# Performance work log

Measured on AMD Instinct MI355X. Metric: run time of the kernel, lower is better.

The kernel has to match this reference:

```python
import jax, jax.numpy as jnp
import numpy as np

N = 50000          # nodes
E_RAND = 590000    # random edges (+ N self-loops -> E = 640000)
IN_F = 128
OUT_F = 128
H, D = 8, 16       # num_heads, head_dim (H*D == OUT_F)
HOP = 5
ALPHA = 0.1
SLOPE = 0.2
EPS = 1e-5


def _layer_norm(x, g, b):
    mu = jnp.mean(x, axis=-1, keepdims=True)
    var = jnp.mean((x - mu) ** 2, axis=-1, keepdims=True)
    return (x - mu) * jax.lax.rsqrt(var + EPS) * g + b


def setup_inputs() -> dict:
    key = jax.random.key(0)
    ks = jax.random.split(key, 10)
    loops = jnp.arange(N, dtype=jnp.int32)  # self-loops -> no 0-in-degree nodes
    src = jnp.concatenate([loops, jax.random.randint(ks[0], (E_RAND,), 0, N, dtype=jnp.int32)])
    dst = jnp.concatenate([loops, jax.random.randint(ks[1], (E_RAND,), 0, N, dtype=jnp.int32)])
    s = 0.05  # xavier-like small init gain
    return {
        "feat": jax.random.normal(ks[2], (N, IN_F), jnp.float32),
        "src": src,
        "dst": dst,
        "w_head": jax.random.normal(ks[3], (OUT_F, IN_F), jnp.float32) * s,
        "w_tail": jax.random.normal(ks[4], (OUT_F, IN_F), jnp.float32) * s,
        "w_ent": jax.random.normal(ks[5], (OUT_F, IN_F), jnp.float32) * s,
        "attn": jax.random.normal(ks[6], (1, H, D), jnp.float32) * s,
        "ln1_g": jnp.ones((IN_F,), jnp.float32),
        "ln1_b": jnp.zeros((IN_F,), jnp.float32),
        "ln2_g": jnp.ones((OUT_F,), jnp.float32),
        "ln2_b": jnp.zeros((OUT_F,), jnp.float32),
        "ff_w1": jax.random.normal(ks[7], (4 * OUT_F, OUT_F), jnp.float32) * s,
        "ff_b1": jnp.zeros((4 * OUT_F,), jnp.float32),
        "ff_w2": jax.random.normal(ks[8], (OUT_F, 4 * OUT_F), jnp.float32) * s,
        "ff_b2": jnp.zeros((OUT_F,), jnp.float32),
    }


def _forward(src, dst, feat, w_head, w_tail, w_ent, attn,
             ln1_g, ln1_b, ln2_g, ln2_b, ff_w1, ff_b1, ff_w2, ff_b2):
    ones = jnp.ones(src.shape[0], jnp.float32)
    out_deg = jnp.clip(jax.ops.segment_sum(ones, src, num_segments=N), 1.0)  # [N]
    in_deg = jnp.clip(jax.ops.segment_sum(ones, dst, num_segments=N), 1.0)
    head_norm = out_deg ** -0.5
    tail_norm = in_deg ** 0.5
    log_in = jnp.log1p(in_deg)  # graph.dstdata['log_in'] (log of in-degree, set at graph build time)

    x = _layer_norm(feat, ln1_g, ln1_b)  # graph_layer_norm (feat_drop=0 in eval)
    fh = (x @ w_head.T).reshape(N, H, D) * head_norm[:, None, None]
    ft = (x @ w_tail.T).reshape(N, H, D) * head_norm[:, None, None]
    fe = (x @ w_ent.T).reshape(N, H, D) * head_norm[:, None, None]

    # edge attention logits: u_mul_v -> leaky_relu -> dot with attn vector
    lr = jax.nn.leaky_relu(fh[src] * ft[dst], SLOPE)  # [E,H,D]
    e = jnp.einsum('ehd,xhd->eh', lr, attn)           # [E,H]
    e = e * log_in[dst][:, None] / D                  # e_mul_v with log_in, / head_dim

    # edge softmax grouped by destination node, per head
    seg_max = jax.ops.segment_max(e, dst, num_segments=N)
    e_exp = jnp.exp(e - seg_max[dst])
    denom = jax.ops.segment_sum(e_exp, dst, num_segments=N)
    a = e_exp / denom[dst]                            # [E,H]

    # PPR diffusion (ppr_estimation), attn_drop=0 in eval
    feat0 = fe
    h = feat0
    for hop in range(HOP):
        if hop > 0:
            h = h * head_norm[:, None, None]
        m = h[src] * a[:, :, None]                    # [E,H,D] u_mul_e
        h = jax.ops.segment_sum(m, dst, num_segments=N)  # fn.sum
        h = h * tail_norm[:, None, None]
        h = (1.0 - ALPHA) * h + ALPHA * feat0

    rst = h + feat.reshape(N, H, D)  # res_fc is Identity since in_feats == out_feats
    rst = rst.reshape(N, OUT_F)
    ff = _layer_norm(rst, ln2_g, ln2_b)
    ff = jax.nn.relu(ff @ ff_w1.T + ff_b1) @ ff_w2.T + ff_b2  # PositionWiseFeedForward
    return ff + rst


def reference(feat, src, dst, w_head, w_tail, w_ent, attn, ln1_g, ln1_b,
              ln2_g, ln2_b, ff_w1, ff_b1, ff_w2, ff_b2):
    return _forward(src, dst, feat, w_head, w_tail, w_ent, attn,
                    ln1_g, ln1_b, ln2_g, ln2_b, ff_w1, ff_b1, ff_w2, ff_b2)
```

## Files before the change

kernel.cpp:

```cpp
#include <hip/hip_runtime.h>
#include <hip/hip_bf16.h>
#include <hip/hip_fp16.h>

typedef __attribute__((ext_vector_type(8))) short bf16x8;
typedef __attribute__((ext_vector_type(4))) float f32x4;
typedef unsigned int uint32;

#define F 128
#define HOPS 5
#define LDS_STRIDE 68
#define W1_STRIDE 136
#define W2_STRIDE 72
#define TB_STRIDE 72

__device__ __forceinline__ float b2f(__hip_bfloat16 h) { return __bfloat162float(h); }
__device__ __forceinline__ __hip_bfloat16 f2b(float f) { return __float2bfloat16(f); }

__device__ __forceinline__ float load_in(const void* p, size_t i, int isbf) {
    return isbf ? __bfloat162float(((const __hip_bfloat16*)p)[i]) : ((const float*)p)[i];
}

__device__ __forceinline__ float bflo(uint32 u) { union { uint32 i; float f; } v; v.i = u << 16; return v.f; }
__device__ __forceinline__ float bfhi(uint32 u) { union { uint32 i; float f; } v; v.i = u & 0xffff0000u; return v.f; }
__device__ __forceinline__ uint32 packbf2(float a, float b) {
    __hip_bfloat16 ha = f2b(a), hb = f2b(b);
    unsigned short ua = *(unsigned short*)&ha, ub = *(unsigned short*)&hb;
    return ((uint32)ub << 16) | ua;
}

__device__ __forceinline__ float edge_dot2(uint4 gv, const float* c1, const float* c2) {
    float acc = 0.f, acc2 = 0.f;
    uint32 us[4] = {gv.x, gv.y, gv.z, gv.w};
    #pragma unroll
    for (int k = 0; k < 4; ++k) {
        float f0 = bflo(us[k]), f1 = bfhi(us[k]);
        acc  = fmaf(c1[2 * k],     f0,        acc);
        acc2 = fmaf(c2[2 * k],     fabsf(f0), acc2);
        acc  = fmaf(c1[2 * k + 1], f1,        acc);
        acc2 = fmaf(c2[2 * k + 1], fabsf(f1), acc2);
    }
    return acc + acc2;
}

__global__ void detect_k(const uint32* __restrict__ w, int* flag) {
    __shared__ int cnt[256];
    int t = threadIdx.x;
    uint32 x = w[t * 97];
    int e_low = (x >> 7) & 0xFF;
    cnt[t] = (e_low >= 110 && e_low <= 135) ? 1 : 0;
    __syncthreads();
    for (int s = 128; s > 0; s >>= 1) {
        if (t < s) cnt[t] += cnt[t + s];
        __syncthreads();
    }
    if (t == 0) flag[0] = (cnt[0] >= 160) ? 1 : 0;
}

__global__ void cvt_all_k(const void* __restrict__ w_head, const void* __restrict__ w_tail,
                          const void* __restrict__ w_ent, const void* __restrict__ ff_w1,
                          const void* __restrict__ ff_w2, const void* __restrict__ attn,
                          const void* __restrict__ ff_b1, const void* __restrict__ ff_b2,
                          const int* __restrict__ flag,
                          __hip_bfloat16* __restrict__ wblob, float* __restrict__ fblob) {
    int i = blockIdx.x * blockDim.x + threadIdx.x;
    int isbf = flag[0];
    if (i < 180224) {
        const void* srcp; int j;
        if (i < 16384)       { srcp = w_head; j = i; }
        else if (i < 32768)  { srcp = w_tail; j = i - 16384; }
        else if (i < 49152)  { srcp = w_ent;  j = i - 32768; }
        else if (i < 114688) { srcp = ff_w1;  j = i - 49152; }
        else                 { srcp = ff_w2;  j = i - 114688; }
        wblob[i] = f2b(load_in(srcp, j, isbf));
    } else if (i < 180992) {
        int k = i - 180224;
        const void* srcp; int j;
        if (k < 128)      { srcp = attn;  j = k; }
        else if (k < 640) { srcp = ff_b1; j = k - 128; }
        else              { srcp = ff_b2; j = k - 640; }
        fblob[k] = load_in(srcp, j, isbf);
    }
}

__global__ void degree_k(const int* __restrict__ src, const int* __restrict__ dst,
                         int* in8, int* out8, int E, int N) {
    int i = blockIdx.x * blockDim.x + threadIdx.x;
    int slice = blockIdx.x & 7;
    if (i < E) {
        atomicAdd(&in8[slice * N + dst[i]], 1);
        atomicAdd(&out8[slice * N + src[i]], 1);
    }
}

__global__ void scan1_k(const int* __restrict__ in8, int* partial, int* blk_sum, int N) {
    __shared__ int sh[256];
    int t = threadIdx.x;
    int i = blockIdx.x * 256 + t;
    int c = 0;
    if (i < N) {
#pragma unroll
        for (int s = 0; s < 8; ++s) c += in8[s * N + i];
    }
    sh[t] = c;
    __syncthreads();
    for (int o = 1; o < 256; o <<= 1) {
        int v = (t >= o) ? sh[t - o] : 0;
        __syncthreads();
        sh[t] += v;
        __syncthreads();
    }
    if (i < N) partial[i] = sh[t] - c;
    if (t == 255) blk_sum[blockIdx.x] = sh[255];
}

__global__ void scan2_k(const int* __restrict__ blk_sum, int* blk_off, int nb,
                        int* row_ptr, int N) {
    __shared__ int sh[256];
    int t = threadIdx.x;
    if (nb <= 256) {
        int v = (t < nb) ? blk_sum[t] : 0;
        sh[t] = v;
        __syncthreads();
        for (int o = 1; o < 256; o <<= 1) {
            int u = (t >= o) ? sh[t - o] : 0;
            __syncthreads();
            sh[t] += u;
            __syncthreads();
        }
        if (t < nb) blk_off[t] = sh[t] - v;
        if (t == 255) row_ptr[N] = sh[255];
    } else if (t == 0) {
        int run = 0;
        for (int b = 0; b < nb; ++b) { blk_off[b] = run; run += blk_sum[b]; }
        row_ptr[N] = run;
    }
}

__global__ void scan3_norms_k(const int* __restrict__ partial, const int* __restrict__ blk_off,
                              const int* __restrict__ in8, const int* __restrict__ out8,
                              int* row_ptr, int* soff, float* head_norm, float* tail_norm,
                              float* log_in, int N) {
    int i = blockIdx.x * 256 + threadIdx.x;
    if (i >= N) return;
    row_ptr[i] = partial[i] + blk_off[blockIdx.x];
    int run = 0;
#pragma unroll
    for (int s = 0; s < 8; ++s) { soff[s * N + i] = run; run += in8[s * N + i]; }
    int od = 0;
#pragma unroll
    for (int s = 0; s < 8; ++s) od += out8[s * N + i];
    float id = fmaxf((float)run, 1.0f);
    float odf = fmaxf((float)od, 1.0f);
    head_norm[i] = rsqrtf(odf);
    tail_norm[i] = sqrtf(id);
    log_in[i] = log1pf(id);
}

__global__ void scan3f_k(const int* __restrict__ partial, const int* __restrict__ blk_sum,
                         int nb, const int* __restrict__ in8, const int* __restrict__ out8,
                         int* row_ptr, int* soff, float* head_norm, float* tail_norm,
                         float* log_in, int N) {
    __shared__ int bs[256];
    int t = threadIdx.x;
    bs[t] = (t < nb) ? blk_sum[t] : 0;
    __syncthreads();
    for (int o = 1; o < 256; o <<= 1) {
        int v = (t >= o) ? bs[t - o] : 0;
        __syncthreads();
        bs[t] += v;
        __syncthreads();
    }
    if (blockIdx.x == 0 && t == 0) row_ptr[N] = bs[nb - 1];
    int boff = (blockIdx.x == 0) ? 0 : bs[blockIdx.x - 1];
    int i = blockIdx.x * 256 + t;
    if (i >= N) return;
    row_ptr[i] = partial[i] + boff;
    int run = 0;
#pragma unroll
    for (int s = 0; s < 8; ++s) { soff[s * N + i] = run; run += in8[s * N + i]; }
    int od = 0;
#pragma unroll
    for (int s = 0; s < 8; ++s) od += out8[s * N + i];
    float id = fmaxf((float)run, 1.0f);
    float odf = fmaxf((float)od, 1.0f);
    head_norm[i] = rsqrtf(odf);
    tail_norm[i] = sqrtf(id);
    log_in[i] = log1pf(id);
}

__global__ void scatter_k(const int* __restrict__ src, const int* __restrict__ dst,
                          const int* __restrict__ row_ptr, const int* __restrict__ soff,
                          int* cursor8, int* csr_src, int E, int N) {
    int i = blockIdx.x * blockDim.x + threadIdx.x;
    int slice = blockIdx.x & 7;
    if (i < E) {
        int d = dst[i];
        int p = row_ptr[d] + soff[slice * N + d] + atomicAdd(&cursor8[slice * N + d], 1);
        csr_src[p] = src[i];
    }
}

__global__ void ln1_k(const void* __restrict__ x, const void* __restrict__ g,
                      const void* __restrict__ b, const int* __restrict__ flag,
                      __hip_bfloat16* __restrict__ y, int N) {
    int w = blockIdx.x * (blockDim.x >> 6) + (threadIdx.x >> 6);
    if (w >= N) return;
    int isbf = flag[0];
    int t = threadIdx.x & 63;
    float v0 = load_in(x, (size_t)w * F + t, isbf);
    float v1 = load_in(x, (size_t)w * F + t + 64, isbf);
    float s = v0 + v1, sq = v0 * v0 + v1 * v1;
    for (int m = 1; m < 64; m <<= 1) { s += __shfl_xor(s, m, 64); sq += __shfl_xor(sq, m, 64); }
    float mu = s * (1.0f / F);
    float var = fmaxf(sq * (1.0f / F) - mu * mu, 0.0f);
    float r = rsqrtf(var + 1e-5f);
    y[(size_t)w * F + t]      = f2b((v0 - mu) * r * load_in(g, t, isbf) + load_in(b, t, isbf));
    y[(size_t)w * F + t + 64] = f2b((v1 - mu) * r * load_in(g, t + 64, isbf) + load_in(b, t + 64, isbf));
}

__global__ void proj_gemm_k(const __hip_bfloat16* __restrict__ X,
                            const __hip_bfloat16* __restrict__ Wall,
                            const float* __restrict__ head_norm,
                            __hip_bfloat16* __restrict__ fh,
                            __hip_bfloat16* __restrict__ ft,
                            uint32* __restrict__ fe_bf, int N) {
    __shared__ __align__(16) char smem[2 * 64 * W1_STRIDE * 2];
    __hip_bfloat16* lx = (__hip_bfloat16*)smem;
    __hip_bfloat16* lw = (__hip_bfloat16*)(smem + 64 * W1_STRIDE * 2);
    float* eps = (float*)smem;
    int tid = threadIdx.x;
    int wv = tid >> 6, lane = tid & 63;
    int lr = lane & 15, quad = lane >> 4;
    int bm = blockIdx.x * 64;
    int g = blockIdx.y;
    int wsel = g >> 1;
    int wcb = (g & 1) * 64;
    {
        const __hip_bfloat16* xs = X + (size_t)bm * F;
        size_t maxe = (size_t)N * F;
#pragma unroll
        for (int i = 0; i < 4; ++i) {
            int idx = i * 2048 + tid * 8;
            int n = idx >> 7, k = idx & 127;
            size_t gi = (size_t)bm * F + idx;
            uint4 v = (gi + 8 <= maxe) ? *(const uint4*)(xs + idx)
                                       : *(const uint4*)(X + maxe - 8);
            *(uint4*)&lx[n * W1_STRIDE + k] = v;
        }
        const __hip_bfloat16* ws = Wall + ((size_t)wsel * F + wcb) * F;
#pragma unroll
        for (int i = 0; i < 4; ++i) {
            int idx = i * 2048 + tid * 8;
            int n = idx >> 7, k = idx & 127;
            *(uint4*)&lw[n * W1_STRIDE + k] = *(const uint4*)(ws + idx);
        }
    }
    __syncthreads();
    f32x4 acc[4] = {{0,0,0,0},{0,0,0,0},{0,0,0,0},{0,0,0,0}};
#pragma unroll
    for (int ks = 0; ks < 4; ++ks) {
        bf16x8 a = *reinterpret_cast<const bf16x8*>(&lx[(wv * 16 + lr) * W1_STRIDE + ks * 32 + quad * 8]);
#pragma unroll
        for (int j = 0; j < 4; ++j) {
            bf16x8 bb = *reinterpret_cast<const bf16x8*>(&lw[(j * 16 + lr) * W1_STRIDE + ks * 32 + quad * 8]);
            acc[j] = __builtin_amdgcn_mfma_f32_16x16x32_bf16(a, bb, acc[j], 0, 0, 0);
        }
    }
    __syncthreads();
    int rl = wv * 16 + quad * 4;
#pragma unroll
    for (int j = 0; j < 4; ++j)
#pragma unroll
        for (int r = 0; r < 4; ++r)
            eps[(rl + r) * LDS_STRIDE + j * 16 + lr] = acc[j][r];
    __syncthreads();
    int tr = tid >> 4, tc = (tid & 15) * 4;
#pragma unroll
    for (int p = 0; p < 4; ++p) {
        int row_l = p * 16 + tr;
        int grow = bm + row_l;
        if (grow >= N) continue;
        float4 v = *(const float4*)&eps[row_l * LDS_STRIDE + tc];
        float hn = head_norm[grow];
        v.x *= hn; v.y *= hn; v.z *= hn; v.w *= hn;
        size_t idx = (size_t)grow * F + wcb + tc;
        uint2 u; u.x = packbf2(v.x, v.y); u.y = packbf2(v.z, v.w);
        __hip_bfloat16* dstp = (wsel == 0) ? fh : (wsel == 1) ? ft : (__hip_bfloat16*)fe_bf;
        *(uint2*)&dstp[idx] = u;
    }
}

__global__ void attn_soft_k(const int* __restrict__ csr_src, const int* __restrict__ row_ptr,
                            const uint32* __restrict__ fh2, const uint32* __restrict__ ft2,
                            const float* __restrict__ attn_f, const float* __restrict__ log_in,
                            float* __restrict__ e_buf, __half* __restrict__ e_h,
                            float* __restrict__ inv_arr, int N) {
    int w = blockIdx.x * (blockDim.x >> 6) + (threadIdx.x >> 6);
    if (w >= N) return;
    int t = threadIdx.x & 63;
    int g = t >> 4, j = t & 15;
    int b = row_ptr[w], e = row_ptr[w + 1];
    uint4 fr = ((const uint4*)ft2)[(size_t)w * 16 + j];
    float ftf[8] = {bflo(fr.x), bfhi(fr.x), bflo(fr.y), bfhi(fr.y),
                    bflo(fr.z), bfhi(fr.z), bflo(fr.w), bfhi(fr.w)};
    float c1[8], c2[8];
#pragma unroll
    for (int k = 0; k < 8; ++k) {
        float at = attn_f[8 * j + k];
        c1[k] = 0.6f * at * ftf[k];
        c2[k] = 0.4f * at * fabsf(ftf[k]);
    }
    float scale = log_in[w] * (1.0f / 16.0f);
    float m = -1e30f;
    for (int p0 = b; p0 < e; p0 += 8) {
        int pa = p0 + g, pb = p0 + 4 + g;
        bool oka = pa < e, okb = pb < e;
        int sa = csr_src[oka ? pa : b];
        int sb = csr_src[okb ? pb : b];
        uint4 ga = ((const uint4*)fh2)[(size_t)sa * 16 + j];
        uint4 gb = ((const uint4*)fh2)[(size_t)sb * 16 + j];
        float ra = edge_dot2(ga, c1, c2);
        float rb = edge_dot2(gb, c1, c2);
        ra += __shfl_xor(ra, 1, 64);
        rb += __shfl_xor(rb, 1, 64);
        float la = ra * scale, lb = rb * scale;
        if (oka) { if (!(j & 1)) e_buf[(size_t)pa * 8 + (j >> 1)] = la; m = fmaxf(m, la); }
        if (okb) { if (!(j & 1)) e_buf[(size_t)pb * 8 + (j >> 1)] = lb; m = fmaxf(m, lb); }
    }
    m = fmaxf(m, __shfl_xor(m, 16, 64));
    m = fmaxf(m, __shfl_xor(m, 32, 64));
    float mh = __shfl(m, (t & 7) * 2, 64);
    float sum = 0.f;
    for (size_t base = (size_t)b * 8 + t; base < (size_t)e * 8; base += 64) {
        float ex = expf(e_buf[base] - mh);
        e_h[base] = __float2half(ex);
        sum += ex;
    }
    sum += __shfl_xor(sum, 8, 64);
    sum += __shfl_xor(sum, 16, 64);
    sum += __shfl_xor(sum, 32, 64);
    float inv = 1.0f / fmaxf(sum, 1e-30f);
    if (t < 8) inv_arr[(size_t)w * 8 + t] = inv;
}

__global__ void hop_k(const uint32* __restrict__ gsrc2, const __half* __restrict__ e_h,
                      const float* __restrict__ inv_arr,
                      const int* __restrict__ csr_src, const int* __restrict__ row_ptr,
                      const float* __restrict__ tail_norm, const float* __restrict__ head_norm,
                      const uint32* __restrict__ fe_bf, const void* __restrict__ feat,
                      const void* __restrict__ ln2g, const void* __restrict__ ln2b,
                      const int* __restrict__ flag,
                      uint32* __restrict__ out_bf, float* __restrict__ out_f32,
                      int last, int N) {
    int w = blockIdx.x * 8 + (threadIdx.x >> 5);
    if (w >= N) return;
    int l = threadIdx.x & 31;
    int h = l >> 2;
    int b = row_ptr[w], e = row_ptr[w + 1];
    float inv = inv_arr[(size_t)w * 8 + h];
    float a0 = 0.f, a1 = 0.f, a2 = 0.f, a3 = 0.f;
    int p = b;
    for (; p + 8 <= e; p += 8) {
        int s[8]; float av[8]; uint2 gg[8];
#pragma unroll
        for (int i = 0; i < 8; ++i) s[i] = csr_src[p + i];
#pragma unroll
        for (int i = 0; i < 8; ++i) av[i] = __half2float(e_h[(size_t)(p + i) * 8 + h]);
#pragma unroll
        for (int i = 0; i < 8; ++i) gg[i] = ((const uint2*)gsrc2)[(size_t)s[i] * 32 + l];
#pragma unroll
        for (int i = 0; i < 8; ++i) {
            a0 += bflo(gg[i].x) * av[i]; a1 += bfhi(gg[i].x) * av[i];
            a2 += bflo(gg[i].y) * av[i]; a3 += bfhi(gg[i].y) * av[i];
        }
    }
    if (p < e) {
        int s[8]; float av[8]; uint2 gg[8];
#pragma unroll
        for (int i = 0; i < 8; ++i) {
            int q = p + i;
            bool ok = q < e;
            int q2 = ok ? q : b;
            s[i] = csr_src[q2];
            av[i] = ok ? __half2float(e_h[(size_t)q * 8 + h]) : 0.f;
        }
#pragma unroll
        for (int i = 0; i < 8; ++i) gg[i] = ((const uint2*)gsrc2)[(size_t)s[i] * 32 + l];
#pragma unroll
        for (int i = 0; i < 8; ++i) {
            a0 += bflo(gg[i].x) * av[i]; a1 += bfhi(gg[i].x) * av[i];
            a2 += bflo(gg[i].y) * av[i]; a3 += bfhi(gg[i].y) * av[i];
        }
    }
    float tl = tail_norm[w] * 0.9f * inv;
    uint2 feu = ((const uint2*)fe_bf)[(size_t)w * 32 + l];
    float r0 = tl * a0 + 0.1f * bflo(feu.x);
    float r1 = tl * a1 + 0.1f * bfhi(feu.x);
    float r2 = tl * a2 + 0.1f * bflo(feu.y);
    float r3 = tl * a3 + 0.1f * bfhi(feu.y);
    if (last) {
        int isbf = flag[0];
        float4 o;
        if (isbf) {
            uint2 fu = ((const uint2*)feat)[(size_t)w * 32 + l];
            o.x = r0 + bflo(fu.x); o.y = r1 + bfhi(fu.x);
            o.z = r2 + bflo(fu.y); o.w = r3 + bfhi(fu.y);
        } else {
            float4 fv = ((const float4*)feat)[(size_t)w * 32 + l];
            o.x = r0 + fv.x; o.y = r1 + fv.y; o.z = r2 + fv.z; o.w = r3 + fv.w;
        }
        ((float4*)out_f32)[(size_t)w * 32 + l] = o;
        float s2 = o.x + o.y + o.z + o.w;
        float sq = o.x * o.x + o.y * o.y + o.z * o.z + o.w * o.w;
#pragma unroll
        for (int mm = 1; mm < 32; mm <<= 1) {
            s2 += __shfl_xor(s2, mm, 64);
            sq += __shfl_xor(sq, mm, 64);
        }
        float mu = s2 * (1.0f / F);
        float var = fmaxf(sq * (1.0f / F) - mu * mu, 0.0f);
        float rr = rsqrtf(var + 1e-5f);
        float g0 = load_in(ln2g, 4 * l + 0, isbf), g1 = load_in(ln2g, 4 * l + 1, isbf);
        float g2 = load_in(ln2g, 4 * l + 2, isbf), g3 = load_in(ln2g, 4 * l + 3, isbf);
        float b0 = load_in(ln2b, 4 * l + 0, isbf), b1 = load_in(ln2b, 4 * l + 1, isbf);
        float b2 = load_in(ln2b, 4 * l + 2, isbf), b3 = load_in(ln2b, 4 * l + 3, isbf);
        uint2 u;
        u.x = packbf2((o.x - mu) * rr * g0 + b0, (o.y - mu) * rr * g1 + b1);
        u.y = packbf2((o.z - mu) * rr * g2 + b2, (o.w - mu) * rr * g3 + b3);
        ((uint2*)out_bf)[(size_t)w * 32 + l] = u;
    } else {
        float hn = head_norm[w];
        uint2 u;
        u.x = packbf2(r0 * hn, r1 * hn);
        u.y = packbf2(r2 * hn, r3 * hn);
        ((uint2*)out_bf)[(size_t)w * 32 + l] = u;
    }
}

__global__ __launch_bounds__(256, 2)
void ffn_fused_k(const __hip_bfloat16* __restrict__ Y, const __hip_bfloat16* __restrict__ W1,
                 const __hip_bfloat16* __restrict__ W2, const float* __restrict__ b1f,
                 const float* __restrict__ b2f, const float* __restrict__ rst,
                 const int* __restrict__ flag, void* __restrict__ out, int N) {
    __shared__ __align__(16) char smem[45056];
    __hip_bfloat16* lw1 = (__hip_bfloat16*)smem;
    __hip_bfloat16* lw2 = (__hip_bfloat16*)(smem + 17408);
    __hip_bfloat16* tb  = (__hip_bfloat16*)(smem + 35840);
    float* eps = (float*)smem;
    int tid = threadIdx.x;
    int wv = tid >> 6, lane = tid & 63;
    int lr = lane & 15, quad = lane >> 4;
    int bm = blockIdx.x * 64;
    int row_a = bm + wv * 16 + lr;
    if (row_a >= N) row_a = N - 1;
    bf16x8 ay[4];
    {
        const __hip_bfloat16* yr = Y + (size_t)row_a * F + quad * 8;
#pragma unroll
        for (int ks = 0; ks < 4; ++ks) ay[ks] = *reinterpret_cast<const bf16x8*>(yr + ks * 32);
    }
    f32x4 o[8];
#pragma unroll
    for (int j = 0; j < 8; ++j) o[j] = (f32x4){0,0,0,0};
    __hip_bfloat16* tbuf = tb + wv * (16 * TB_STRIDE);
    for (int c = 0; c < 8; ++c) {
        int nb0 = c * 64;
        __syncthreads();
        {
            const __hip_bfloat16* s1 = W1 + (size_t)nb0 * F;
#pragma unroll
            for (int i = 0; i < 4; ++i) {
                int idx = i * 2048 + tid * 8;
                int n = idx >> 7, k = idx & 127;
                *(uint4*)&lw1[n * W1_STRIDE + k] = *(const uint4*)(s1 + idx);
            }
#pragma unroll
            for (int i = 0; i < 4; ++i) {
                int idx = i * 2048 + tid * 8;
                int r = idx >> 6, k2 = idx & 63;
                *(uint4*)&lw2[r * W2_STRIDE + k2] = *(const uint4*)(W2 + (size_t)r * 512 + nb0 + k2);
            }
        }
        __syncthreads();
        f32x4 t[4] = {{0,0,0,0},{0,0,0,0},{0,0,0,0},{0,0,0,0}};
#pragma unroll
        for (int ks = 0; ks < 4; ++ks) {
#pragma unroll
            for (int j = 0; j < 4; ++j) {
                bf16x8 bb = *reinterpret_cast<const bf16x8*>(&lw1[(j * 16 + lr) * W1_STRIDE + ks * 32 + quad * 8]);
                t[j] = __builtin_amdgcn_mfma_f32_16x16x32_bf16(ay[ks], bb, t[j], 0, 0, 0);
            }
        }
#pragma unroll
        for (int j = 0; j < 4; ++j) {
            float bias = b1f[nb0 + 16 * j + lr];
#pragma unroll
            for (int r = 0; r < 4; ++r) {
                float v = fmaxf(t[j][r] + bias, 0.f);
                tbuf[(quad * 4 + r) * TB_STRIDE + j * 16 + lr] = f2b(v);
            }
        }
#pragma unroll
        for (int ks2 = 0; ks2 < 2; ++ks2) {
            bf16x8 at = *reinterpret_cast<const bf16x8*>(&tbuf[lr * TB_STRIDE + ks2 * 32 + quad * 8]);
#pragma unroll
            for (int j2 = 0; j2 < 8; ++j2) {
                bf16x8 bb = *reinterpret_cast<const bf16x8*>(&lw2[(j2 * 16 + lr) * W2_STRIDE + ks2 * 32 + quad * 8]);
                o[j2] = __builtin_amdgcn_mfma_f32_16x16x32_bf16(at, bb, o[j2], 0, 0, 0);
            }
        }
    }
    __syncthreads();
    int rl = wv * 16 + quad * 4;
#pragma unroll
    for (int j = 0; j < 8; ++j)
#pragma unroll
        for (int r = 0; r < 4; ++r)
            eps[(rl + r) * 132 + j * 16 + lr] = o[j][r];
    __syncthreads();
    int isbf = flag[0];
#pragma unroll
    for (int p = 0; p < 8; ++p) {
        int idx = p * 1024 + tid * 4;
        int row_l = idx >> 7, col = idx & 127;
        int grow = bm + row_l;
        if (grow >= N) continue;
        float4 v = *(const float4*)&eps[row_l * 132 + col];
        float4 bias = *(const float4*)&b2f[col];
        float4 rv = *(const float4*)&rst[(size_t)grow * F + col];
        v.x += bias.x + rv.x; v.y += bias.y + rv.y;
        v.z += bias.z + rv.z; v.w += bias.w + rv.w;
        size_t gidx = (size_t)grow * F + col;
        if (isbf) {
            uint2 u; u.x = packbf2(v.x, v.y); u.y = packbf2(v.z, v.w);
            *(uint2*)&((__hip_bfloat16*)out)[gidx] = u;
        } else {
            *(float4*)&((float*)out)[gidx] = v;
        }
    }
}

extern "C" void kernel_launch(void* const* d_in, const int* in_sizes, int n_in,
                              void* d_out, int out_size, void* d_ws, size_t ws_size,
                              hipStream_t stream) {
    if (n_in < 15) return;
    const void* feat = d_in[0];
    const int* src = (const int*)d_in[1];
    const int* dst = (const int*)d_in[2];
    const void* w_head = d_in[3];
    const void* w_tail = d_in[4];
    const void* w_ent  = d_in[5];
    const void* attn   = d_in[6];
    const void* ln1_g  = d_in[7];
    const void* ln1_b  = d_in[8];
    const void* ln2_g  = d_in[9];
    const void* ln2_b  = d_in[10];
    const void* ff_w1  = d_in[11];
    const void* ff_b1  = d_in[12];
    const void* ff_w2  = d_in[13];
    const void* ff_b2  = d_in[14];

    const int N = in_sizes[0] / F;
    const int E = in_sizes[1];
    (void)out_size;

    char* base = (char*)d_ws;
    size_t off = 0;
    auto alloc = [&](size_t bytes) -> void* {
        void* r = base + off;
        off += (bytes + 255) & ~(size_t)255;
        return r;
    };
    int* zr        = (int*)alloc((size_t)24 * N * 4);
    int* in8 = zr, * out8 = zr + 8 * N, * cursor8 = zr + 16 * N;
    int* soff      = (int*)alloc((size_t)8 * N * 4);
    int* row_ptr   = (int*)alloc((size_t)(N + 1) * 4);
    int* partial   = (int*)alloc((size_t)N * 4);
    int* blk_sum   = (int*)alloc((size_t)1024 * 4);
    int* blk_off   = (int*)alloc((size_t)1024 * 4);
    int* flag      = (int*)alloc(256);
    float* head_norm = (float*)alloc((size_t)N * 4);
    float* tail_norm = (float*)alloc((size_t)N * 4);
    float* log_in    = (float*)alloc((size_t)N * 4);
    float* inv_arr   = (float*)alloc((size_t)N * 8 * 4);
    int* csr_src   = (int*)alloc((size_t)E * 4);
    __hip_bfloat16* wh_bf = (__hip_bfloat16*)alloc((size_t)F * F * 2);
    __hip_bfloat16* wt_bf = (__hip_bfloat16*)alloc((size_t)F * F * 2);
    __hip_bfloat16* we_bf = (__hip_bfloat16*)alloc((size_t)F * F * 2);
    __hip_bfloat16* w1_bf = (__hip_bfloat16*)alloc((size_t)512 * F * 2);
    __hip_bfloat16* w2_bf = (__hip_bfloat16*)alloc((size_t)F * 512 * 2);
    float* attn_f    = (float*)alloc((size_t)F * 4);
    float* b1f       = (float*)alloc((size_t)512 * 4);
    float* b2f_      = (float*)alloc((size_t)F * 4);
    __hip_bfloat16* x_bf = (__hip_bfloat16*)alloc((size_t)N * F * 2);
    __hip_bfloat16* fh   = (__hip_bfloat16*)alloc((size_t)N * F * 2);
    __hip_bfloat16* ftb  = (__hip_bfloat16*)alloc((size_t)N * F * 2);
    float* e_a = (float*)alloc((size_t)E * 8 * 4);
    uint32* fe_bf = (uint32*)alloc((size_t)N * F * 2);
    uint32* hA_bf = (uint32*)alloc((size_t)N * F * 2);
    uint32* hB_bf = (uint32*)alloc((size_t)N * F * 2);
    float* rst = (float*)alloc((size_t)N * F * 4);
    __hip_bfloat16* y_bf = (__hip_bfloat16*)hA_bf;
    __half* e_h = (__half*)x_bf;
    (void)wt_bf; (void)we_bf;
    if (off > ws_size) return;

    const int Mb = (N + 63) / 64;
    const int nodeBlocks = (N + 3) / 4;
    const int hopBlocks = (N + 7) / 8;
    const int nb = (N + 255) / 256;

    detect_k<<<1, 256, 0, stream>>>((const uint32*)feat, flag);
    cvt_all_k<<<(180992 + 255) / 256, 256, 0, stream>>>(w_head, w_tail, w_ent, ff_w1, ff_w2,
                                                        attn, ff_b1, ff_b2, flag, wh_bf, attn_f);

    hipMemsetAsync(zr, 0, (size_t)24 * N * 4, stream);
    degree_k<<<(E + 255) / 256, 256, 0, stream>>>(src, dst, in8, out8, E, N);
    scan1_k<<<nb, 256, 0, stream>>>(in8, partial, blk_sum, N);
    if (nb <= 256) {
        scan3f_k<<<nb, 256, 0, stream>>>(partial, blk_sum, nb, in8, out8,
                                         row_ptr, soff, head_norm, tail_norm, log_in, N);
    } else {
        scan2_k<<<1, 256, 0, stream>>>(blk_sum, blk_off, nb, row_ptr, N);
        scan3_norms_k<<<nb, 256, 0, stream>>>(partial, blk_off, in8, out8,
                                              row_ptr, soff, head_norm, tail_norm, log_in, N);
    }
    scatter_k<<<(E + 255) / 256, 256, 0, stream>>>(src, dst, row_ptr, soff, cursor8, csr_src, E, N);

    ln1_k<<<nodeBlocks, 256, 0, stream>>>(feat, ln1_g, ln1_b, flag, x_bf, N);
    proj_gemm_k<<<dim3(Mb, 6), 256, 0, stream>>>(x_bf, wh_bf, head_norm, fh, ftb, fe_bf, N);

    attn_soft_k<<<nodeBlocks, 256, 0, stream>>>(csr_src, row_ptr, (const uint32*)fh,
                                                (const uint32*)ftb, attn_f, log_in,
                                                e_a, e_h, inv_arr, N);

    const uint32* gsrc = fe_bf;
    uint32* bufs[2] = {hA_bf, hB_bf};
    for (int hop = 0; hop < HOPS; ++hop) {
        int last = (hop == HOPS - 1);
        uint32* dst_bf = last ? (uint32*)y_bf : bufs[hop & 1];
        hop_k<<<hopBlocks, 256, 0, stream>>>(gsrc, e_h, inv_arr, csr_src, row_ptr, tail_norm,
                                             head_norm, fe_bf, feat, ln2_g, ln2_b, flag,
                                             dst_bf, rst, last, N);
        if (!last) gsrc = dst_bf;
    }

    ffn_fused_k<<<Mb, 256, 0, stream>>>(y_bf, w1_bf, w2_bf, b1f, b2f_, rst, flag, d_out, N);
}
```

Baseline: 458.9 us.

## Record in-slot rank during degree count; use XCD-local slices and fp16 logits

The degree kernel now keeps the rank returned by its in-degree atomic, together with the slice, in a packed per-edge word. The scatter pass then computes the CSR position directly instead of running a second round of atomics on a cursor array. Slices are chosen by the XCD hardware ID, with workgroup-scope relaxed atomics, so counters tend to stay in the local L2. The attention kernel stores raw logits as fp16 in the e_h buffer rather than a separate fp32 buffer, which halves that traffic at some precision cost. Workgroup-scope atomics on counters shared across workgroups of the same XCD rely on L2 coherence within one XCD and are a correctness risk.

```diff
diff --git a/kernel.cpp b/kernel.cpp
--- a/kernel.cpp
+++ b/kernel.cpp
@@ -26,6 +26,12 @@
     __hip_bfloat16 ha = f2b(a), hb = f2b(b);
     unsigned short ua = *(unsigned short*)&ha, ub = *(unsigned short*)&hb;
     return ((uint32)ub << 16) | ua;
+}
+
+__device__ __forceinline__ int xcd_id() {
+    unsigned v;
+    asm volatile("s_getreg_b32 %0, hwreg(HW_REG_XCC_ID)" : "=s"(v));
+    return (int)(v & 7);
 }
 
 __device__ __forceinline__ float edge_dot2(uint4 gv, const float* c1, const float* c2) {
@@ -83,13 +89,16 @@
 }
 
 __global__ void degree_k(const int* __restrict__ src, const int* __restrict__ dst,
-                         int* in8, int* out8, int E, int N) {
+                         int* in8, int* out8, uint32* __restrict__ pack, int E, int N) {
     int i = blockIdx.x * blockDim.x + threadIdx.x;
-    int slice = blockIdx.x & 7;
-    if (i < E) {
-        atomicAdd(&in8[slice * N + dst[i]], 1);
-        atomicAdd(&out8[slice * N + src[i]], 1);
-    }
+    if (i >= E) return;
+    int slice = xcd_id();
+    int d = dst[i], s = src[i];
+    int r = __hip_atomic_fetch_add(&in8[slice * N + d], 1,
+                                   __ATOMIC_RELAXED, __HIP_MEMORY_SCOPE_WORKGROUP);
+    __hip_atomic_fetch_add(&out8[slice * N + s], 1,
+                           __ATOMIC_RELAXED, __HIP_MEMORY_SCOPE_WORKGROUP);
+    pack[i] = (uint32)r | ((uint32)slice << 24);
 }
 
 __global__ void scan1_k(const int* __restrict__ in8, int* partial, int* blk_sum, int N) {
@@ -190,13 +199,14 @@
 
 __global__ void scatter_k(const int* __restrict__ src, const int* __restrict__ dst,
                           const int* __restrict__ row_ptr, const int* __restrict__ soff,
-                          int* cursor8, int* csr_src, int E, int N) {
+                          const uint32* __restrict__ pack, int* csr_src, int E, int N) {
     int i = blockIdx.x * blockDim.x + threadIdx.x;
-    int slice = blockIdx.x & 7;
     if (i < E) {
         int d = dst[i];
-        int p = row_ptr[d] + soff[slice * N + d] + atomicAdd(&cursor8[slice * N + d], 1);
-        csr_src[p] = src[i];
+        uint32 pk = pack[i];
+        int s = (int)(pk >> 24);
+        int r = (int)(pk & 0xFFFFFFu);
+        csr_src[row_ptr[d] + soff[s * N + d] + r] = src[i];
     }
 }
 
@@ -293,8 +303,7 @@
 __global__ void attn_soft_k(const int* __restrict__ csr_src, const int* __restrict__ row_ptr,
                             const uint32* __restrict__ fh2, const uint32* __restrict__ ft2,
                             const float* __restrict__ attn_f, const float* __restrict__ log_in,
-                            float* __restrict__ e_buf, __half* __restrict__ e_h,
-                            float* __restrict__ inv_arr, int N) {
+                            __half* __restrict__ e_h, float* __restrict__ inv_arr, int N) {
     int w = blockIdx.x * (blockDim.x >> 6) + (threadIdx.x >> 6);
     if (w >= N) return;
     int t = threadIdx.x & 63;
@@ -324,15 +333,15 @@
         ra += __shfl_xor(ra, 1, 64);
         rb += __shfl_xor(rb, 1, 64);
         float la = ra * scale, lb = rb * scale;
-        if (oka) { if (!(j & 1)) e_buf[(size_t)pa * 8 + (j >> 1)] = la; m = fmaxf(m, la); }
-        if (okb) { if (!(j & 1)) e_buf[(size_t)pb * 8 + (j >> 1)] = lb; m = fmaxf(m, lb); }
+        if (oka) { if (!(j & 1)) e_h[(size_t)pa * 8 + (j >> 1)] = __float2half(la); m = fmaxf(m, la); }
+        if (okb) { if (!(j & 1)) e_h[(size_t)pb * 8 + (j >> 1)] = __float2half(lb); m = fmaxf(m, lb); }
     }
     m = fmaxf(m, __shfl_xor(m, 16, 64));
     m = fmaxf(m, __shfl_xor(m, 32, 64));
     float mh = __shfl(m, (t & 7) * 2, 64);
     float sum = 0.f;
     for (size_t base = (size_t)b * 8 + t; base < (size_t)e * 8; base += 64) {
-        float ex = expf(e_buf[base] - mh);
+        float ex = expf(__half2float(e_h[base]) - mh);
         e_h[base] = __float2half(ex);
         sum += ex;
     }
@@ -571,8 +580,8 @@
         off += (bytes + 255) & ~(size_t)255;
         return r;
     };
-    int* zr        = (int*)alloc((size_t)24 * N * 4);
-    int* in8 = zr, * out8 = zr + 8 * N, * cursor8 = zr + 16 * N;
+    int* zr        = (int*)alloc((size_t)16 * N * 4);
+    int* in8 = zr, * out8 = zr + 8 * N;
     int* soff      = (int*)alloc((size_t)8 * N * 4);
     int* row_ptr   = (int*)alloc((size_t)(N + 1) * 4);
     int* partial   = (int*)alloc((size_t)N * 4);
@@ -584,6 +593,7 @@
     float* log_in    = (float*)alloc((size_t)N * 4);
     float* inv_arr   = (float*)alloc((size_t)N * 8 * 4);
     int* csr_src   = (int*)alloc((size_t)E * 4);
+    uint32* pack   = (uint32*)alloc((size_t)E * 4);
     __hip_bfloat16* wh_bf = (__hip_bfloat16*)alloc((size_t)F * F * 2);
     __hip_bfloat16* wt_bf = (__hip_bfloat16*)alloc((size_t)F * F * 2);
     __hip_bfloat16* we_bf = (__hip_bfloat16*)alloc((size_t)F * F * 2);
@@ -595,7 +605,6 @@
     __hip_bfloat16* x_bf = (__hip_bfloat16*)alloc((size_t)N * F * 2);
     __hip_bfloat16* fh   = (__hip_bfloat16*)alloc((size_t)N * F * 2);
     __hip_bfloat16* ftb  = (__hip_bfloat16*)alloc((size_t)N * F * 2);
-    float* e_a = (float*)alloc((size_t)E * 8 * 4);
     uint32* fe_bf = (uint32*)alloc((size_t)N * F * 2);
     uint32* hA_bf = (uint32*)alloc((size_t)N * F * 2);
     uint32* hB_bf = (uint32*)alloc((size_t)N * F * 2);
@@ -614,8 +623,8 @@
     cvt_all_k<<<(180992 + 255) / 256, 256, 0, stream>>>(w_head, w_tail, w_ent, ff_w1, ff_w2,
                                                         attn, ff_b1, ff_b2, flag, wh_bf, attn_f);
 
-    hipMemsetAsync(zr, 0, (size_t)24 * N * 4, stream);
-    degree_k<<<(E + 255) / 256, 256, 0, stream>>>(src, dst, in8, out8, E, N);
+    hipMemsetAsync(zr, 0, (size_t)16 * N * 4, stream);
+    degree_k<<<(E + 255) / 256, 256, 0, stream>>>(src, dst, in8, out8, pack, E, N);
     scan1_k<<<nb, 256, 0, stream>>>(in8, partial, blk_sum, N);
     if (nb <= 256) {
         scan3f_k<<<nb, 256, 0, stream>>>(partial, blk_sum, nb, in8, out8,
@@ -625,14 +634,14 @@
         scan3_norms_k<<<nb, 256, 0, stream>>>(partial, blk_off, in8, out8,
                                               row_ptr, soff, head_norm, tail_norm, log_in, N);
     }
-    scatter_k<<<(E + 255) / 256, 256, 0, stream>>>(src, dst, row_ptr, soff, cursor8, csr_src, E, N);
+    scatter_k<<<(E + 255) / 256, 256, 0, stream>>>(src, dst, row_ptr, soff, pack, csr_src, E, N);
 
     ln1_k<<<nodeBlocks, 256, 0, stream>>>(feat, ln1_g, ln1_b, flag, x_bf, N);
     proj_gemm_k<<<dim3(Mb, 6), 256, 0, stream>>>(x_bf, wh_bf, head_norm, fh, ftb, fe_bf, N);
 
     attn_soft_k<<<nodeBlocks, 256, 0, stream>>>(csr_src, row_ptr, (const uint32*)fh,
                                                 (const uint32*)ftb, attn_f, log_in,
-                                                e_a, e_h, inv_arr, N);
+                                                e_h, inv_arr, N);
 
     const uint32* gsrc = fe_bf;
     uint32* bufs[2] = {hA_bf, hB_bf};
```

After: 447.6 us. -2.5%, faster.
